# Performance work log

Hardware: AMD Instinct MI355X
Metric: run time of the kernel (lower is better)

## Reference

```python
import jax, jax.numpy as jnp
import numpy as np

N_NODES = 50000
N_EDGES = 800000
IN_DIM = 64
OUT_DIM = 64
EDGE_DIM = 16
LN_EPS = 1e-5


def setup_inputs() -> dict:
    key = jax.random.key(0)
    ks = jax.random.split(key, 12)
    def lin(k, fan_in, fan_out):
        # torch nn.Linear default init: U(-1/sqrt(fan_in), 1/sqrt(fan_in))
        kw, kb = jax.random.split(k)
        bound = 1.0 / np.sqrt(fan_in)
        W = jax.random.uniform(kw, (fan_in, fan_out), jnp.float32, -bound, bound)
        b = jax.random.uniform(kb, (fan_out,), jnp.float32, -bound, bound)
        return W, b
    x = jax.random.normal(ks[0], (N_NODES, IN_DIM), jnp.float32)
    edge_index = jax.random.randint(ks[1], (2, N_EDGES), 0, N_NODES, jnp.int64 if jax.config.jax_enable_x64 else jnp.int32)
    edge_features = jax.random.normal(ks[2], (N_EDGES, EDGE_DIM), jnp.float32)
    W1, b1 = lin(ks[3], IN_DIM + EDGE_DIM, OUT_DIM)   # msg_mlp layer 1
    W2, b2 = lin(ks[4], OUT_DIM, OUT_DIM)             # msg_mlp layer 2
    W3, b3 = lin(ks[5], IN_DIM + OUT_DIM, OUT_DIM)    # update_mlp
    gamma = jnp.ones((OUT_DIM,), jnp.float32)
    beta = jnp.zeros((OUT_DIM,), jnp.float32)
    return {"x": x, "edge_index": edge_index, "edge_features": edge_features,
            "W1": W1, "b1": b1, "W2": W2, "b2": b2, "W3": W3, "b3": b3,
            "gamma": gamma, "beta": beta}


def reference(x, edge_index, edge_features, W1, b1, W2, b2, W3, b3, gamma, beta):
    num_nodes = x.shape[0]
    src, dst = edge_index[0], edge_index[1]
    # gather source node feats, concat with edge feats -> message MLP
    msg_in = jnp.concatenate([x[src], edge_features], axis=-1)           # [E, in+edge]
    h = jax.nn.relu(msg_in @ W1 + b1)
    messages = h @ W2 + b2                                               # [E, out]
    # scatter-add aggregate + mean by in-degree (count + 1e-8)
    agg = jax.ops.segment_sum(messages, dst, num_segments=num_nodes)     # [N, out]
    cnt = jax.ops.segment_sum(jnp.ones((messages.shape[0],), x.dtype), dst,
                              num_segments=num_nodes)[:, None]           # [N, 1]
    agg = agg / (cnt + 1e-8)
    # update MLP + residual (Identity since in_dim == out_dim) + LayerNorm
    updated = jax.nn.relu(jnp.concatenate([x, agg], axis=-1) @ W3 + b3)  # [N, out]
    y = updated + x
    mu = jnp.mean(y, axis=-1, keepdims=True)
    var = jnp.var(y, axis=-1, keepdims=True)
    return (y - mu) * jax.lax.rsqrt(var + LN_EPS) * gamma + beta
```

## Files before the change

### kernel.cpp

```cpp
#include <hip/hip_runtime.h>

typedef unsigned short u16;
typedef unsigned int u32;
typedef short short8 __attribute__((ext_vector_type(8)));
typedef short short4v __attribute__((ext_vector_type(4)));
typedef float floatx4 __attribute__((ext_vector_type(4)));

#define NE 800000
#define NNODES 50000
#define NBLK 196

#define EDGE_GRID 1280

#define LDS_FENCE() __asm__ volatile("s_waitcnt lgkmcnt(0)" ::: "memory")

__device__ __forceinline__ u16 f2bf(float f) {
    union { float f; unsigned int i; } v; v.f = f;
    return (u16)((v.i + 0x7fffu + ((v.i >> 16) & 1u)) >> 16);
}
__device__ __forceinline__ float bf2f(u16 u) {
    union { unsigned int i; float f; } v; v.i = ((unsigned int)u) << 16; return v.f;
}
__device__ __forceinline__ short8 pack8(const float4 a, const float4 b) {
    short8 o;
    o[0] = (short)f2bf(a.x); o[1] = (short)f2bf(a.y);
    o[2] = (short)f2bf(a.z); o[3] = (short)f2bf(a.w);
    o[4] = (short)f2bf(b.x); o[5] = (short)f2bf(b.y);
    o[6] = (short)f2bf(b.z); o[7] = (short)f2bf(b.w);
    return o;
}
__device__ __forceinline__ short8 ld8_bf(const float* __restrict__ p) {
    return pack8(*(const float4*)p, *(const float4*)(p + 4));
}

#define MFMA16(a, b, c) __builtin_amdgcn_mfma_f32_16x16x32_bf16(a, b, c, 0, 0, 0)

__global__ __launch_bounds__(256) void prep_kernel(
    const float* __restrict__ x, const int* __restrict__ ei,
    int* __restrict__ hist, u16* __restrict__ xbf)
{
    const int id = blockIdx.x * 256 + threadIdx.x;
    if (id < NE) atomicAdd(&hist[ei[NE + id]], 1);
    if (id < NNODES * 8) {
        *(short8*)&xbf[(size_t)id * 8] = ld8_bf(x + (size_t)id * 8);
    }
}

__global__ __launch_bounds__(256) void scan1_kernel(
    const int* __restrict__ hist, int* __restrict__ cursor, int* __restrict__ bsum)
{
    const int i = blockIdx.x * 256 + threadIdx.x;
    const int lane = threadIdx.x & 63;
    const int w = threadIdx.x >> 6;
    const int v = (i < NNODES) ? hist[i] : 0;
    int inc = v;
    #pragma unroll
    for (int o = 1; o < 64; o <<= 1) {
        const int tt = __shfl_up(inc, o);
        if (lane >= o) inc += tt;
    }
    __shared__ int ws[4];
    if (lane == 63) ws[w] = inc;
    __syncthreads();
    int add = 0;
    for (int j = 0; j < w; ++j) add += ws[j];
    const int excl = inc - v + add;
    if (i < NNODES) cursor[i] = excl;
    if (threadIdx.x == 255) bsum[blockIdx.x] = excl + v;
}

__global__ __launch_bounds__(256) void scan2_kernel(
    const int* __restrict__ bsum, int* __restrict__ bsumx)
{
    const int tid = threadIdx.x;
    const int lane = tid & 63;
    const int w = tid >> 6;
    const int v = (tid < NBLK) ? bsum[tid] : 0;
    int inc = v;
    #pragma unroll
    for (int o = 1; o < 64; o <<= 1) {
        const int tt = __shfl_up(inc, o);
        if (lane >= o) inc += tt;
    }
    __shared__ int ws[4];
    if (lane == 63) ws[w] = inc;
    __syncthreads();
    int add = 0;
    for (int j = 0; j < w; ++j) add += ws[j];
    bsumx[tid] = inc - v + add;
}

__global__ __launch_bounds__(256) void scatter_kernel(
    const int* __restrict__ ei, int* __restrict__ cursor,
    const int* __restrict__ bsumx, uint2* __restrict__ sde)
{
    const int e = blockIdx.x * 256 + threadIdx.x;
    if (e < NE) {
        const int dst = ei[NE + e];
        const int p = atomicAdd(&cursor[dst], 1) + bsumx[dst >> 8];
        uint2 v;
        v.x = (u32)e;
        v.y = ((u32)ei[e] << 16) | (u32)dst;
        sde[p] = v;
    }
}

__global__ __launch_bounds__(256) void edge_kernel(
    const u16* __restrict__ xbf, const float* __restrict__ ef,
    const float* __restrict__ w1, const float* __restrict__ b1,
    const float* __restrict__ w2, const float* __restrict__ b2,
    const uint2* __restrict__ sde, float* __restrict__ agg)
{
    constexpr int S1 = 104;
    constexpr int S2 = 72;
    __shared__ u16 A1[4][16 * S1];
    __shared__ u16 Hs[4][16 * S2];
    __shared__ int Ds[4][16];
    __shared__ u16 W2f[2][4][64 * 8];

    const int wid  = threadIdx.x >> 6;
    const int lane = threadIdx.x & 63;
    const int q    = lane >> 4;
    const int c    = lane & 15;
    const int r4   = lane >> 2;
    const int p4   = lane & 3;

    short8 w1f[3][4];
    #pragma unroll
    for (int kk = 0; kk < 3; ++kk)
        #pragma unroll
        for (int nn = 0; nn < 4; ++nn)
            #pragma unroll
            for (int j = 0; j < 8; ++j) {
                const int k = kk * 32 + q * 8 + j;
                w1f[kk][nn][j] = (k < 80) ? (short)f2bf(w1[k * 64 + nn * 16 + c]) : (short)0;
            }
    if (wid == 0) {
        #pragma unroll
        for (int kk = 0; kk < 2; ++kk)
            #pragma unroll
            for (int nn = 0; nn < 4; ++nn) {
                short8 f;
                #pragma unroll
                for (int j = 0; j < 8; ++j) {
                    const int k = kk * 32 + q * 8 + j;
                    f[j] = (short)f2bf(w2[k * 64 + nn * 16 + c]);
                }
                *(short8*)&W2f[kk][nn][lane * 8] = f;
            }
    }
    float b1v[4], b2v[4];
    #pragma unroll
    for (int nn = 0; nn < 4; ++nn) {
        b1v[nn] = b1[nn * 16 + c];
        b2v[nn] = b2[nn * 16 + c];
    }
    if (q == 1) {
        const short8 z8 = {0, 0, 0, 0, 0, 0, 0, 0};
        *(short8*)&A1[wid][c * S1 + 80] = z8;
        *(short8*)&A1[wid][c * S1 + 88] = z8;
    }
    __syncthreads();

    const floatx4 zero = {0.f, 0.f, 0.f, 0.f};
    const int ntile = NE / 16;
    const int stride = gridDim.x * 4;
    int t = blockIdx.x * 4 + wid;

    uint2 sdB; u32 eB;
    short8 xa, xb; float4 ev;
    int dcur;
    {
        const uint2 sdA = sde[t * 16 + c];
        const u32  eA  = sde[t * 16 + r4].x;
        dcur = (int)(sdA.y & 0xffffu);
        const int sA = (int)(sdA.y >> 16);
        int tb = t + stride; if (tb >= ntile) tb = ntile - 1;
        sdB = sde[tb * 16 + c];
        eB  = sde[tb * 16 + r4].x;
        const u16* xp = xbf + (size_t)sA * 64 + q * 16;
        xa = *(const short8*)xp;
        xb = *(const short8*)(xp + 8);
        ev = *(const float4*)(ef + (size_t)eA * 16 + p4 * 4);
    }

    for (; t < ntile; t += stride) {
        u16* arow = &A1[wid][c * S1 + q * 16];
        *(short8*)arow       = xa;
        *(short8*)(arow + 8) = xb;
        {
            short4v e4;
            e4[0] = (short)f2bf(ev.x); e4[1] = (short)f2bf(ev.y);
            e4[2] = (short)f2bf(ev.z); e4[3] = (short)f2bf(ev.w);
            *(short4v*)&A1[wid][r4 * S1 + 64 + p4 * 4] = e4;
        }
        if (q == 0) Ds[wid][c] = dcur;
        LDS_FENCE();

        short8 a1k[3];
        #pragma unroll
        for (int kk = 0; kk < 3; ++kk)
            a1k[kk] = *(const short8*)&A1[wid][c * S1 + kk * 32 + q * 8];

        const int dnext = (int)(sdB.y & 0xffffu);
        {
            const int sN = (int)(sdB.y >> 16);
            const u16* xp = xbf + (size_t)sN * 64 + q * 16;
            xa = *(const short8*)xp;
            xb = *(const short8*)(xp + 8);
            ev = *(const float4*)(ef + (size_t)eB * 16 + p4 * 4);
        }
        {
            int tb = t + 2 * stride; if (tb >= ntile) tb = ntile - 1;
            sdB = sde[tb * 16 + c];
            eB  = sde[tb * 16 + r4].x;
        }

        #pragma unroll
        for (int nn = 0; nn < 4; ++nn) {
            floatx4 acc = MFMA16(a1k[0], w1f[0][nn], zero);
            acc = MFMA16(a1k[1], w1f[1][nn], acc);
            acc = MFMA16(a1k[2], w1f[2][nn], acc);
            #pragma unroll
            for (int r = 0; r < 4; ++r) {
                const float h = fmaxf(acc[r] + b1v[nn], 0.f);
                Hs[wid][(q * 4 + r) * S2 + nn * 16 + c] = f2bf(h);
            }
        }
        LDS_FENCE();

        short8 a2k[2];
        #pragma unroll
        for (int kk = 0; kk < 2; ++kk)
            a2k[kk] = *(const short8*)&Hs[wid][c * S2 + kk * 32 + q * 8];

        #pragma unroll
        for (int nn = 0; nn < 4; ++nn) {
            const short8 wf0 = *(const short8*)&W2f[0][nn][lane * 8];
            const short8 wf1 = *(const short8*)&W2f[1][nn][lane * 8];
            floatx4 mg = MFMA16(a2k[0], wf0, zero);
            mg = MFMA16(a2k[1], wf1, mg);
            #pragma unroll
            for (int r = 0; r < 4; ++r)
                Hs[wid][(q * 4 + r) * S2 + nn * 16 + c] = f2bf(mg[r] + b2v[nn]);
        }
        LDS_FENCE();

        int dc = Ds[wid][0];
        float acc = bf2f(Hs[wid][lane]);
        #pragma unroll
        for (int row = 1; row < 16; ++row) {
            const int d = Ds[wid][row];
            const float v = bf2f(Hs[wid][row * S2 + lane]);
            if (d == dc) {
                acc += v;
            } else {
                atomicAdd(&agg[(size_t)dc * 64 + lane], acc);
                dc = d;
                acc = v;
            }
        }
        atomicAdd(&agg[(size_t)dc * 64 + lane], acc);

        dcur = dnext;
    }
}

__global__ __launch_bounds__(256) void node_kernel(
    const u16* __restrict__ xbf, const float* __restrict__ w3,
    const float* __restrict__ b3, const float* __restrict__ g,
    const float* __restrict__ bb, const float* __restrict__ agg,
    const int* __restrict__ hist, float* __restrict__ out)
{
    constexpr int S3 = 136;
    __shared__ u16 Cs[4][16 * S3];

    const int wid  = threadIdx.x >> 6;
    const int lane = threadIdx.x & 63;
    const int q    = lane >> 4;
    const int c    = lane & 15;

    short8 w3f[4][4];
    #pragma unroll
    for (int kk = 0; kk < 4; ++kk)
        #pragma unroll
        for (int nn = 0; nn < 4; ++nn)
            #pragma unroll
            for (int j = 0; j < 8; ++j) {
                const int k = kk * 32 + q * 8 + j;
                w3f[kk][nn][j] = (short)f2bf(w3[k * 64 + nn * 16 + c]);
            }
    float b3v[4], gv[4], bv[4];
    #pragma unroll
    for (int nn = 0; nn < 4; ++nn) {
        b3v[nn] = b3[nn * 16 + c];
        gv[nn]  = g[nn * 16 + c];
        bv[nn]  = bb[nn * 16 + c];
    }

    const floatx4 zero = {0.f, 0.f, 0.f, 0.f};
    const int ntile = NNODES / 16;

    for (int t = blockIdx.x * 4 + wid; t < ntile; t += gridDim.x * 4) {
        const int n0 = t * 16;
        const int node = n0 + c;
        u16* crow = &Cs[wid][c * S3];

        if (q < 2) {
            const u16* xp = xbf + (size_t)node * 64 + q * 32;
            *(short8*)&crow[q * 32]      = *(const short8*)xp;
            *(short8*)&crow[q * 32 + 8]  = *(const short8*)(xp + 8);
            *(short8*)&crow[q * 32 + 16] = *(const short8*)(xp + 16);
            *(short8*)&crow[q * 32 + 24] = *(const short8*)(xp + 24);
        } else {
            const int p = q - 2;
            const float inv = 1.0f / ((float)hist[node] + 1e-8f);
            const float* ap = agg + (size_t)node * 64 + p * 32;
            #pragma unroll
            for (int gi = 0; gi < 4; ++gi) {
                const float4 v0 = *(const float4*)(ap + gi * 8);
                const float4 v1 = *(const float4*)(ap + gi * 8 + 4);
                short8 o;
                o[0] = (short)f2bf(v0.x * inv);
                o[1] = (short)f2bf(v0.y * inv);
                o[2] = (short)f2bf(v0.z * inv);
                o[3] = (short)f2bf(v0.w * inv);
                o[4] = (short)f2bf(v1.x * inv);
                o[5] = (short)f2bf(v1.y * inv);
                o[6] = (short)f2bf(v1.z * inv);
                o[7] = (short)f2bf(v1.w * inv);
                *(short8*)&crow[64 + p * 32 + gi * 8] = o;
            }
        }
        LDS_FENCE();

        short8 af[4];
        #pragma unroll
        for (int kk = 0; kk < 4; ++kk)
            af[kk] = *(const short8*)&Cs[wid][c * S3 + kk * 32 + q * 8];

        float y[4][4];
        float s[4]  = {0.f, 0.f, 0.f, 0.f};
        float ss[4] = {0.f, 0.f, 0.f, 0.f};
        #pragma unroll
        for (int nn = 0; nn < 4; ++nn) {
            floatx4 acc = MFMA16(af[0], w3f[0][nn], zero);
            acc = MFMA16(af[1], w3f[1][nn], acc);
            acc = MFMA16(af[2], w3f[2][nn], acc);
            acc = MFMA16(af[3], w3f[3][nn], acc);
            #pragma unroll
            for (int r = 0; r < 4; ++r) {
                const float upd = fmaxf(acc[r] + b3v[nn], 0.f);
                const float xv = bf2f(Cs[wid][(q * 4 + r) * S3 + nn * 16 + c]);
                const float yy = upd + xv;
                y[r][nn] = yy;
                s[r] += yy;
                ss[r] += yy * yy;
            }
        }

        #pragma unroll
        for (int r = 0; r < 4; ++r) {
            float sr = s[r], sq = ss[r];
            #pragma unroll
            for (int off = 1; off < 16; off <<= 1) {
                sr += __shfl_xor(sr, off);
                sq += __shfl_xor(sq, off);
            }
            const float mu  = sr * (1.0f / 64.0f);
            const float var = sq * (1.0f / 64.0f) - mu * mu;
            const float rs  = rsqrtf(var + 1e-5f);
            float* op = out + (size_t)(n0 + q * 4 + r) * 64 + c;
            #pragma unroll
            for (int nn = 0; nn < 4; ++nn)
                op[nn * 16] = (y[r][nn] - mu) * rs * gv[nn] + bv[nn];
        }
    }
}

extern "C" void kernel_launch(void* const* d_in, const int* in_sizes, int n_in,
                              void* d_out, int out_size, void* d_ws, size_t ws_size,
                              hipStream_t stream) {
    const float* x   = (const float*)d_in[0];
    const int*   ei  = (const int*)d_in[1];
    const float* ef  = (const float*)d_in[2];
    const float* w1  = (const float*)d_in[3];
    const float* b1  = (const float*)d_in[4];
    const float* w2  = (const float*)d_in[5];
    const float* b2  = (const float*)d_in[6];
    const float* w3  = (const float*)d_in[7];
    const float* b3  = (const float*)d_in[8];
    const float* g   = (const float*)d_in[9];
    const float* bb  = (const float*)d_in[10];

    float* agg   = (float*)d_ws;
    int* hist    = (int*)d_ws + 3200000;
    int* cursor  = hist + NNODES;
    int* bsum    = cursor + NNODES;
    int* bsumx   = bsum + 256;
    u16* xbf     = (u16*)(bsumx + 256);
    uint2* sde   = (uint2*)((int*)d_ws + 4900512);

    hipMemsetAsync(d_ws, 0, (size_t)(3200000 + NNODES) * sizeof(float), stream);
    prep_kernel<<<3125, 256, 0, stream>>>(x, ei, hist, xbf);
    scan1_kernel<<<NBLK, 256, 0, stream>>>(hist, cursor, bsum);
    scan2_kernel<<<1, 256, 0, stream>>>(bsum, bsumx);
    scatter_kernel<<<3125, 256, 0, stream>>>(ei, cursor, bsumx, sde);
    edge_kernel<<<EDGE_GRID, 256, 0, stream>>>(xbf, ef, w1, b1, w2, b2, sde, agg);
    node_kernel<<<782, 256, 0, stream>>>(xbf, w3, b3, g, bb, agg, hist, (float*)d_out);
}
```

Baseline: 291.3 us.

## Merge memset, histogram, scan and scatter into one cooperative kernel

Replaces the memset and four preprocessing launches (histogram plus bf16 cast, two scan passes, scatter) with a single cooperative kernel that uses grid-wide syncs between phases. Zeroing of agg and hist moves into the kernel as grid-stride loops. The aim is to remove per-launch overhead and the idle gaps between small dependent kernels. In exchange it adds four grid barriers, caps parallelism at a fixed 1280-block grid, and relies on cooperative launch residency.

```diff
diff --git a/kernel.cpp b/kernel.cpp
--- a/kernel.cpp
+++ b/kernel.cpp
@@ -1,4 +1,7 @@
 #include <hip/hip_runtime.h>
+#include <hip/hip_cooperative_groups.h>
+
+namespace cg = cooperative_groups;
 
 typedef unsigned short u16;
 typedef unsigned int u32;
@@ -11,6 +14,7 @@
 #define NBLK 196
 
 #define EDGE_GRID 1280
+#define PRE_GRID 1280
 
 #define LDS_FENCE() __asm__ volatile("s_waitcnt lgkmcnt(0)" ::: "memory")
 
@@ -35,67 +39,66 @@
 
 #define MFMA16(a, b, c) __builtin_amdgcn_mfma_f32_16x16x32_bf16(a, b, c, 0, 0, 0)
 
-__global__ __launch_bounds__(256) void prep_kernel(
+__global__ __launch_bounds__(256) void pre_kernel(
     const float* __restrict__ x, const int* __restrict__ ei,
-    int* __restrict__ hist, u16* __restrict__ xbf)
+    float* __restrict__ agg, int* __restrict__ hist, int* __restrict__ cursor,
+    int* __restrict__ bsum, int* __restrict__ bsumx,
+    u16* __restrict__ xbf, uint2* __restrict__ sde)
 {
-    const int id = blockIdx.x * 256 + threadIdx.x;
-    if (id < NE) atomicAdd(&hist[ei[NE + id]], 1);
-    if (id < NNODES * 8) {
-        *(short8*)&xbf[(size_t)id * 8] = ld8_bf(x + (size_t)id * 8);
-    }
-}
-
-__global__ __launch_bounds__(256) void scan1_kernel(
-    const int* __restrict__ hist, int* __restrict__ cursor, int* __restrict__ bsum)
-{
-    const int i = blockIdx.x * 256 + threadIdx.x;
-    const int lane = threadIdx.x & 63;
-    const int w = threadIdx.x >> 6;
-    const int v = (i < NNODES) ? hist[i] : 0;
-    int inc = v;
-    #pragma unroll
-    for (int o = 1; o < 64; o <<= 1) {
-        const int tt = __shfl_up(inc, o);
-        if (lane >= o) inc += tt;
-    }
+    cg::grid_group grid = cg::this_grid();
+    const int tid = blockIdx.x * 256 + threadIdx.x;
+    const int nth = gridDim.x * 256;
     __shared__ int ws[4];
-    if (lane == 63) ws[w] = inc;
-    __syncthreads();
-    int add = 0;
-    for (int j = 0; j < w; ++j) add += ws[j];
-    const int excl = inc - v + add;
-    if (i < NNODES) cursor[i] = excl;
-    if (threadIdx.x == 255) bsum[blockIdx.x] = excl + v;
-}
-
-__global__ __launch_bounds__(256) void scan2_kernel(
-    const int* __restrict__ bsum, int* __restrict__ bsumx)
-{
-    const int tid = threadIdx.x;
-    const int lane = tid & 63;
-    const int w = tid >> 6;
-    const int v = (tid < NBLK) ? bsum[tid] : 0;
-    int inc = v;
-    #pragma unroll
-    for (int o = 1; o < 64; o <<= 1) {
-        const int tt = __shfl_up(inc, o);
-        if (lane >= o) inc += tt;
-    }
-    __shared__ int ws[4];
-    if (lane == 63) ws[w] = inc;
-    __syncthreads();
-    int add = 0;
-    for (int j = 0; j < w; ++j) add += ws[j];
-    bsumx[tid] = inc - v + add;
-}
-
-__global__ __launch_bounds__(256) void scatter_kernel(
-    const int* __restrict__ ei, int* __restrict__ cursor,
-    const int* __restrict__ bsumx, uint2* __restrict__ sde)
-{
-    const int e = blockIdx.x * 256 + threadIdx.x;
-    if (e < NE) {
+
+    for (int i = tid; i < 3200000; i += nth) agg[i] = 0.f;
+    for (int i = tid; i < NNODES; i += nth) hist[i] = 0;
+    grid.sync();
+
+    for (int e = tid; e < NE; e += nth) atomicAdd(&hist[ei[NE + e]], 1);
+    for (int i = tid; i < NNODES * 8; i += nth)
+        *(short8*)&xbf[(size_t)i * 8] = ld8_bf(x + (size_t)i * 8);
+    grid.sync();
+
+    if (blockIdx.x < NBLK) {
+        const int i = blockIdx.x * 256 + threadIdx.x;
+        const int lane = threadIdx.x & 63;
+        const int w = threadIdx.x >> 6;
+        const int v = (i < NNODES) ? hist[i] : 0;
+        int inc = v;
+        #pragma unroll
+        for (int o = 1; o < 64; o <<= 1) {
+            const int tt = __shfl_up(inc, o);
+            if (lane >= o) inc += tt;
+        }
+        if (lane == 63) ws[w] = inc;
+        __syncthreads();
+        int add = 0;
+        for (int j = 0; j < w; ++j) add += ws[j];
+        const int excl = inc - v + add;
+        if (i < NNODES) cursor[i] = excl;
+        if (threadIdx.x == 255) bsum[blockIdx.x] = excl + v;
+    }
+    grid.sync();
+
+    if (blockIdx.x == 0) {
+        const int lane = threadIdx.x & 63;
+        const int w = threadIdx.x >> 6;
+        const int v = (threadIdx.x < NBLK) ? bsum[threadIdx.x] : 0;
+        int inc = v;
+        #pragma unroll
+        for (int o = 1; o < 64; o <<= 1) {
+            const int tt = __shfl_up(inc, o);
+            if (lane >= o) inc += tt;
+        }
+        if (lane == 63) ws[w] = inc;
+        __syncthreads();
+        int add = 0;
+        for (int j = 0; j < w; ++j) add += ws[j];
+        bsumx[threadIdx.x] = inc - v + add;
+    }
+    grid.sync();
+
+    for (int e = tid; e < NE; e += nth) {
         const int dst = ei[NE + e];
         const int p = atomicAdd(&cursor[dst], 1) + bsumx[dst >> 8];
         uint2 v;
@@ -401,11 +404,12 @@
     u16* xbf     = (u16*)(bsumx + 256);
     uint2* sde   = (uint2*)((int*)d_ws + 4900512);
 
-    hipMemsetAsync(d_ws, 0, (size_t)(3200000 + NNODES) * sizeof(float), stream);
-    prep_kernel<<<3125, 256, 0, stream>>>(x, ei, hist, xbf);
-    scan1_kernel<<<NBLK, 256, 0, stream>>>(hist, cursor, bsum);
-    scan2_kernel<<<1, 256, 0, stream>>>(bsum, bsumx);
-    scatter_kernel<<<3125, 256, 0, stream>>>(ei, cursor, bsumx, sde);
+    void* pre_args[] = {
+        (void*)&x, (void*)&ei, (void*)&agg, (void*)&hist, (void*)&cursor,
+        (void*)&bsum, (void*)&bsumx, (void*)&xbf, (void*)&sde
+    };
+    hipLaunchCooperativeKernel((void*)pre_kernel, dim3(PRE_GRID), dim3(256),
+                               pre_args, 0, stream);
     edge_kernel<<<EDGE_GRID, 256, 0, stream>>>(xbf, ef, w1, b1, w2, b2, sde, agg);
     node_kernel<<<782, 256, 0, stream>>>(xbf, w3, b3, g, bb, agg, hist, (float*)d_out);
 }
```

Result: slower. 777.0 us (+166.8%).
